# Kernel tuning notes

Measured on AMD Instinct MI355X. Metric: run time of the kernel, lower is better.

The kernel has to match this reference:

```python
import jax, jax.numpy as jnp
import numpy as np

N_C, N_E, IN_FEAT, OUT_FEAT = 8192, 8192, 256, 128


def setup_inputs() -> dict:
    key = jax.random.key(0)
    ks = jax.random.split(key, 9)
    s = 1.0 / np.sqrt(IN_FEAT)
    return {
        "emb_cause": jax.random.normal(ks[0], (N_C, IN_FEAT), jnp.float32),
        "emb_effect": jax.random.normal(ks[1], (N_E, IN_FEAT), jnp.float32),
        "causal_mask": jax.random.randint(ks[2], (N_C, N_E), 0, 2, jnp.int32),
        "Wq": jax.random.uniform(ks[3], (IN_FEAT, OUT_FEAT), jnp.float32, -s, s),
        "bq": jax.random.uniform(ks[4], (OUT_FEAT,), jnp.float32, -s, s),
        "Wk": jax.random.uniform(ks[5], (IN_FEAT, OUT_FEAT), jnp.float32, -s, s),
        "bk": jax.random.uniform(ks[6], (OUT_FEAT,), jnp.float32, -s, s),
        "Wv": jax.random.uniform(ks[7], (IN_FEAT, OUT_FEAT), jnp.float32, -s, s),
        "bv": jax.random.uniform(ks[8], (OUT_FEAT,), jnp.float32, -s, s),
    }


def reference(emb_cause, emb_effect, causal_mask, Wq, bq, Wk, bk, Wv, bv):
    Q = emb_cause @ Wq + bq          # [N_c, D]
    K = emb_effect @ Wk + bk         # [N_e, D]
    V = emb_effect @ Wv + bv         # [N_e, D]
    scale = 1.0 / jnp.sqrt(jnp.asarray(Q.shape[-1], Q.dtype))
    scores = (Q @ K.T) * scale       # [N_c, N_e]
    scores = jnp.where(causal_mask == 0, -jnp.inf, scores)
    attn_weights = jax.nn.softmax(scores, axis=-1)
    causal_output = attn_weights @ V  # [N_c, D]
    return causal_output, attn_weights
```

## Files before the change

### kernel.cpp

```cpp
#include <hip/hip_runtime.h>

#define NC   8192
#define NEFF 8192
#define DIN  256
#define DOUT 128
#define SCALE 0.08838834764831843f

typedef float  f32x4  __attribute__((ext_vector_type(4)));
typedef short  s16x8  __attribute__((ext_vector_type(8)));
typedef unsigned long long u64;

__device__ __forceinline__ short f2bf(float f) {
    unsigned int u = __builtin_bit_cast(unsigned int, f);
    u += 0x7FFFu + ((u >> 16) & 1u);
    return (short)(u >> 16);
}

__device__ __forceinline__ s16x8 ld8(const short* p) {
    return *(const s16x8*)__builtin_assume_aligned(p, 16);
}

__device__ __forceinline__ unsigned getdw(int4 v, int i) {
    switch (i & 3) {
        case 0: return (unsigned)v.x;
        case 1: return (unsigned)v.y;
        case 2: return (unsigned)v.z;
        default: return (unsigned)v.w;
    }
}


__global__ __launch_bounds__(256) void pack_kernel(
    const int* __restrict__ mask, u64* __restrict__ bm)
{
    const size_t stride = (size_t)gridDim.x * 256;
    const size_t i0 = (size_t)blockIdx.x * 256 + threadIdx.x;
    const bool lead = (threadIdx.x & 63) == 0;
    for (size_t i = i0; i < (size_t)NC * NEFF; i += 8 * stride) {
        int m[8];
#pragma unroll
        for (int j = 0; j < 8; j++) m[j] = mask[i + j * stride];
        u64 b[8];
#pragma unroll
        for (int j = 0; j < 8; j++) b[j] = __ballot(m[j] != 0);
        if (lead) {
#pragma unroll
            for (int j = 0; j < 8; j++) bm[(i + j * stride) >> 6] = b[j];
        }
    }
}

__global__ __launch_bounds__(256, 2) void qkv_kernel(
    const float* __restrict__ embc, const float* __restrict__ embe,
    const float* __restrict__ Wq, const float* __restrict__ bq,
    const float* __restrict__ Wk, const float* __restrict__ bk,
    const float* __restrict__ Wv, const float* __restrict__ bv,
    short* __restrict__ Qf, short* __restrict__ Kf, short* __restrict__ Vf)
{
    const int mat = blockIdx.y;
    const float* src  = (mat == 0) ? embc : embe;
    const float* W    = (mat == 0) ? Wq : (mat == 1 ? Wk : Wv);
    const float* bias = (mat == 0) ? bq : (mat == 1 ? bk : bv);

    __shared__ short wt[DOUT][136];
    __shared__ short tbuf[4][16][132];
    __shared__ short tbufV[128][68];

    const int tid  = threadIdx.x;
    const int wave = tid >> 6, lane = tid & 63;
    const int quad = lane >> 4, ln16 = lane & 15;
    const int rowbase = blockIdx.x * 64;
    const int arow = rowbase + wave * 16 + ln16;

    f32x4 acc[8];
#pragma unroll
    for (int i = 0; i < 8; i++) acc[i] = (f32x4){0.f, 0.f, 0.f, 0.f};

    for (int h = 0; h < 2; h++) {
        __syncthreads();
        {
            const int n0 = (tid & 31) * 4;
            const int kb = tid >> 5;
#pragma unroll
            for (int i = 0; i < 16; i++) {
                const int k = kb + i * 8;
                const float4 w4 = *(const float4*)(W + (size_t)(h * 128 + k) * DOUT + n0);
                wt[n0 + 0][k] = f2bf(w4.x);
                wt[n0 + 1][k] = f2bf(w4.y);
                wt[n0 + 2][k] = f2bf(w4.z);
                wt[n0 + 3][k] = f2bf(w4.w);
            }
        }
        __syncthreads();

        s16x8 afr[4];
#pragma unroll
        for (int kc = 0; kc < 4; kc++) {
            const float* ap = src + (size_t)arow * DIN + h * 128 + kc * 32 + quad * 8;
            const float4 a0 = *(const float4*)ap;
            const float4 a1 = *(const float4*)(ap + 4);
            s16x8 a;
            a[0] = f2bf(a0.x); a[1] = f2bf(a0.y); a[2] = f2bf(a0.z); a[3] = f2bf(a0.w);
            a[4] = f2bf(a1.x); a[5] = f2bf(a1.y); a[6] = f2bf(a1.z); a[7] = f2bf(a1.w);
            afr[kc] = a;
        }
#pragma unroll
        for (int nt = 0; nt < 8; nt++) {
#pragma unroll
            for (int kc = 0; kc < 4; kc++) {
                const s16x8 b = ld8(&wt[nt * 16 + ln16][kc * 32 + quad * 8]);
                acc[nt] = __builtin_amdgcn_mfma_f32_16x16x32_bf16(afr[kc], b, acc[nt], 0, 0, 0);
            }
        }
    }

    if (mat < 2) {
        short* dst = (mat == 0) ? Qf : Kf;
        const float sc = (mat == 0) ? SCALE : 1.0f;
#pragma unroll
        for (int nt = 0; nt < 8; nt++) {
            const float bb = bias[nt * 16 + ln16];
#pragma unroll
            for (int r = 0; r < 4; r++)
                tbuf[wave][quad * 4 + r][nt * 16 + ln16] = f2bf((acc[nt][r] + bb) * sc);
        }
        const int tile = blockIdx.x * 4 + wave;
#pragma unroll
        for (int kc = 0; kc < 4; kc++) {
            const s16x8 fr = ld8(&tbuf[wave][ln16][kc * 32 + quad * 8]);
            *(s16x8*)(dst + ((size_t)(tile * 4 + kc) * 64 + lane) * 8) = fr;
        }
    } else {
#pragma unroll
        for (int nt = 0; nt < 8; nt++) {
            const float bb = bias[nt * 16 + ln16];
#pragma unroll
            for (int r = 0; r < 4; r++)
                tbufV[nt * 16 + ln16][wave * 16 + quad * 4 + r] = f2bf(acc[nt][r] + bb);
        }
        __syncthreads();
        const int ct = blockIdx.x >> 1;
        const int ksub0 = (blockIdx.x & 1) * 2;
        const int ks = wave & 1;
#pragma unroll
        for (int t = 0; t < 4; t++) {
            const int nt2 = (wave >> 1) * 4 + t;
            const s16x8 fr = ld8(&tbufV[nt2 * 16 + ln16][ks * 32 + quad * 8]);
            *(s16x8*)(Vf + ((size_t)((ct * 8 + nt2) * 4 + ksub0 + ks) * 64 + lane) * 8) = fr;
        }
    }
}

__global__ __launch_bounds__(256, 4) void stats_kernel(
    const unsigned int* __restrict__ bm, const short* __restrict__ Qf,
    const short* __restrict__ Kf, float* __restrict__ lsum)
{
    const int bx = blockIdx.x, strip = blockIdx.y;
    const int tid  = threadIdx.x;
    const int wave = tid >> 6, lane = tid & 63;
    const int quad = lane >> 4, ln16 = lane & 15;
    const int rowbase = bx * 128 + wave * 32;
    const int t0 = rowbase >> 4;

    s16x8 aq[2][4];
#pragma unroll
    for (int rs = 0; rs < 2; rs++)
#pragma unroll
        for (int kc = 0; kc < 4; kc++)
            aq[rs][kc] = ld8(Qf + ((size_t)((t0 + rs) * 4 + kc) * 64 + lane) * 8);

    float lp[8] = {0.f, 0.f, 0.f, 0.f, 0.f, 0.f, 0.f, 0.f};

    for (int it = 0; it < 4; it++) {
        const int cb = strip * 512 + it * 128;

        int4 bmv[2][4];
#pragma unroll
        for (int rs = 0; rs < 2; rs++)
#pragma unroll
            for (int r = 0; r < 4; r++)
                bmv[rs][r] = *(const int4*)(bm + (size_t)(rowbase + rs * 16 + quad * 4 + r) * 256 + (cb >> 5));

#pragma unroll
        for (int nt = 0; nt < 8; nt++) {
            s16x8 bq[4];
#pragma unroll
            for (int kc = 0; kc < 4; kc++)
                bq[kc] = ld8(Kf + ((size_t)(((cb >> 4) + nt) * 4 + kc) * 64 + lane) * 8);
            f32x4 c0 = (f32x4){0.f, 0.f, 0.f, 0.f};
            f32x4 c1 = (f32x4){0.f, 0.f, 0.f, 0.f};
#pragma unroll
            for (int kc = 0; kc < 4; kc++) {
                c0 = __builtin_amdgcn_mfma_f32_16x16x32_bf16(aq[0][kc], bq[kc], c0, 0, 0, 0);
                c1 = __builtin_amdgcn_mfma_f32_16x16x32_bf16(aq[1][kc], bq[kc], c1, 0, 0, 0);
            }
#pragma unroll
            for (int rs = 0; rs < 2; rs++)
#pragma unroll
                for (int r = 0; r < 4; r++) {
                    const unsigned d = getdw(bmv[rs][r], nt >> 1);
                    const float cv = rs ? c1[r] : c0[r];
                    if ((d >> ((nt & 1) * 16 + ln16)) & 1u)
                        lp[rs * 4 + r] += __expf(cv);
                }
        }
    }

#pragma unroll
    for (int i = 0; i < 8; i++) {
        float v = lp[i];
        v += __shfl_xor(v, 1); v += __shfl_xor(v, 2);
        v += __shfl_xor(v, 4); v += __shfl_xor(v, 8);
        if (ln16 == 0)
            atomicAdd(&lsum[rowbase + (i >> 2) * 16 + quad * 4 + (i & 3)], v);
    }
}

__global__ __launch_bounds__(256, 4) void attn_kernel(
    const short* __restrict__ Qf, const short* __restrict__ Kf,
    const short* __restrict__ Vf, const float* __restrict__ lsum,
    const unsigned int* __restrict__ bm,
    float* __restrict__ outO, float* __restrict__ outW)
{
    __shared__ short wlds[4][16][132];

    const int bx = blockIdx.x, strip = blockIdx.y;
    const int tid  = threadIdx.x;
    const int wave = tid >> 6, lane = tid & 63;
    const int quad = lane >> 4, ln16 = lane & 15;
    const int rowbase = bx * 64 + wave * 16;
    const int t0 = rowbase >> 4;

    s16x8 aq[4];
#pragma unroll
    for (int kc = 0; kc < 4; kc++)
        aq[kc] = ld8(Qf + ((size_t)(t0 * 4 + kc) * 64 + lane) * 8);

    float rl[4];
#pragma unroll
    for (int r = 0; r < 4; r++)
        rl[r] = 1.0f / lsum[rowbase + quad * 4 + r];

    f32x4 o[8];
#pragma unroll
    for (int i = 0; i < 8; i++) o[i] = (f32x4){0.f, 0.f, 0.f, 0.f};

    for (int it = 0; it < 8; it++) {
        const int cb = strip * 1024 + it * 128;

        int4 bmv[4];
#pragma unroll
        for (int r = 0; r < 4; r++)
            bmv[r] = *(const int4*)(bm + (size_t)(rowbase + quad * 4 + r) * 256 + (cb >> 5));

#pragma unroll
        for (int nt = 0; nt < 8; nt++) {
            s16x8 bq[4];
#pragma unroll
            for (int kc = 0; kc < 4; kc++)
                bq[kc] = ld8(Kf + ((size_t)(((cb >> 4) + nt) * 4 + kc) * 64 + lane) * 8);
            f32x4 c = (f32x4){0.f, 0.f, 0.f, 0.f};
#pragma unroll
            for (int kc = 0; kc < 4; kc++)
                c = __builtin_amdgcn_mfma_f32_16x16x32_bf16(aq[kc], bq[kc], c, 0, 0, 0);
#pragma unroll
            for (int r = 0; r < 4; r++) {
                const int row = rowbase + quad * 4 + r;
                const unsigned d = getdw(bmv[r], nt >> 1);
                const float wv = ((d >> ((nt & 1) * 16 + ln16)) & 1u)
                                     ? __expf(c[r]) * rl[r] : 0.0f;
                outW[(size_t)row * NEFF + cb + nt * 16 + ln16] = wv;
                wlds[wave][quad * 4 + r][nt * 16 + ln16] = f2bf(wv);
            }
        }

#pragma unroll
        for (int ks = 0; ks < 4; ks++) {
            const s16x8 aw = ld8(&wlds[wave][ln16][ks * 32 + quad * 8]);
#pragma unroll
            for (int nt2 = 0; nt2 < 8; nt2++) {
                const s16x8 bv = ld8(Vf + ((size_t)(((cb >> 7) * 8 + nt2) * 4 + ks) * 64 + lane) * 8);
                o[nt2] = __builtin_amdgcn_mfma_f32_16x16x32_bf16(aw, bv, o[nt2], 0, 0, 0);
            }
        }
    }

#pragma unroll
    for (int nt2 = 0; nt2 < 8; nt2++)
#pragma unroll
        for (int r = 0; r < 4; r++) {
            const int row = rowbase + quad * 4 + r;
            atomicAdd(&outO[(size_t)row * DOUT + nt2 * 16 + ln16], o[nt2][r]);
        }
}

extern "C" void kernel_launch(void* const* d_in, const int* in_sizes, int n_in,
                              void* d_out, int out_size, void* d_ws, size_t ws_size,
                              hipStream_t stream) {
    (void)in_sizes; (void)n_in; (void)out_size; (void)ws_size;

    const float* embc = (const float*)d_in[0];
    const float* embe = (const float*)d_in[1];
    const int*   mask = (const int*)d_in[2];
    const float* Wq = (const float*)d_in[3];
    const float* bq = (const float*)d_in[4];
    const float* Wk = (const float*)d_in[5];
    const float* bk = (const float*)d_in[6];
    const float* Wv = (const float*)d_in[7];
    const float* bv = (const float*)d_in[8];

    char* ws = (char*)d_ws;
    short* Qf = (short*)(ws);
    short* Kf = (short*)(ws + (2u << 20));
    short* Vf = (short*)(ws + (4u << 20));
    float* lsum = (float*)(ws + (6u << 20));
    unsigned int* bm = (unsigned int*)(ws + (8u << 20));

    float* outO = (float*)d_out;
    float* outW = outO + (size_t)NC * DOUT;

    hipMemsetAsync(lsum, 0, NC * sizeof(float), stream);
    hipMemsetAsync(outO, 0, (size_t)NC * DOUT * sizeof(float), stream);

    pack_kernel<<<8192, 256, 0, stream>>>(mask, (u64*)bm);
    qkv_kernel<<<dim3(128, 3), 256, 0, stream>>>(embc, embe, Wq, bq, Wk, bk, Wv, bv,
                                                 Qf, Kf, Vf);
    stats_kernel<<<dim3(64, 16), 256, 0, stream>>>(bm, Qf, Kf, lsum);
    attn_kernel<<<dim3(128, 8), 256, 0, stream>>>(Qf, Kf, Vf, lsum, bm, outO, outW);
}
```

Before: 659.9 us.

## Fuse mask bit-packing into stats kernel and drop separate pack pass

Removes the standalone pack_kernel. Each stats block now reads its own 128x512 tile of the int32 mask, ballots it into a bitmask held in LDS, and writes that bitmask to global memory for attn_kernel. It then reads mask bits from LDS instead of global memory. This saves one kernel launch and one extra global round trip of the bitmask, in exchange for more LDS use and a serial packing phase at the start of each stats block.

Result: slower. 751.5 us (+13.9%).

```diff
diff --git a/kernel.cpp b/kernel.cpp
--- a/kernel.cpp
+++ b/kernel.cpp
@@ -29,26 +29,6 @@
     }
 }
 
-
-__global__ __launch_bounds__(256) void pack_kernel(
-    const int* __restrict__ mask, u64* __restrict__ bm)
-{
-    const size_t stride = (size_t)gridDim.x * 256;
-    const size_t i0 = (size_t)blockIdx.x * 256 + threadIdx.x;
-    const bool lead = (threadIdx.x & 63) == 0;
-    for (size_t i = i0; i < (size_t)NC * NEFF; i += 8 * stride) {
-        int m[8];
-#pragma unroll
-        for (int j = 0; j < 8; j++) m[j] = mask[i + j * stride];
-        u64 b[8];
-#pragma unroll
-        for (int j = 0; j < 8; j++) b[j] = __ballot(m[j] != 0);
-        if (lead) {
-#pragma unroll
-            for (int j = 0; j < 8; j++) bm[(i + j * stride) >> 6] = b[j];
-        }
-    }
-}
 
 __global__ __launch_bounds__(256, 2) void qkv_kernel(
     const float* __restrict__ embc, const float* __restrict__ embe,
@@ -152,14 +132,49 @@
 }
 
 __global__ __launch_bounds__(256, 4) void stats_kernel(
-    const unsigned int* __restrict__ bm, const short* __restrict__ Qf,
-    const short* __restrict__ Kf, float* __restrict__ lsum)
+    const int* __restrict__ mask, const short* __restrict__ Qf,
+    const short* __restrict__ Kf, float* __restrict__ lsum,
+    u64* __restrict__ bmG)
 {
+    __shared__ u64 lds_bm[128][8];
+
     const int bx = blockIdx.x, strip = blockIdx.y;
     const int tid  = threadIdx.x;
     const int wave = tid >> 6, lane = tid & 63;
     const int quad = lane >> 4, ln16 = lane & 15;
-    const int rowbase = bx * 128 + wave * 32;
+    const int blkrow = bx * 128;
+    const int cb0 = strip * 512;
+
+    for (int i = 0; i < 256; i += 8) {
+        int mv[8];
+#pragma unroll
+        for (int j = 0; j < 8; j++) {
+            const int t = (i + j) * 4 + wave;
+            mv[j] = mask[(size_t)(blkrow + (t >> 3)) * NEFF + cb0 + (t & 7) * 64 + lane];
+        }
+        u64 lb[8];
+#pragma unroll
+        for (int j = 0; j < 8; j++) lb[j] = __ballot(mv[j] != 0);
+        if (lane == 0) {
+#pragma unroll
+            for (int j = 0; j < 8; j++) {
+                const int t = (i + j) * 4 + wave;
+                lds_bm[t >> 3][t & 7] = lb[j];
+            }
+        }
+    }
+    __syncthreads();
+
+    {
+        const int r = tid >> 1, half = tid & 1;
+        const int4* src = (const int4*)&lds_bm[r][half * 4];
+        int4* dst = (int4*)(bmG + (size_t)(blkrow + r) * 128 + strip * 8 + half * 4);
+        dst[0] = src[0];
+        dst[1] = src[1];
+    }
+
+    const int rowbase = blkrow + wave * 32;
+    const int wrow = wave * 32;
     const int t0 = rowbase >> 4;
 
     s16x8 aq[2][4];
@@ -172,14 +187,15 @@
     float lp[8] = {0.f, 0.f, 0.f, 0.f, 0.f, 0.f, 0.f, 0.f};
 
     for (int it = 0; it < 4; it++) {
-        const int cb = strip * 512 + it * 128;
+        const int cb = cb0 + it * 128;
 
         int4 bmv[2][4];
 #pragma unroll
         for (int rs = 0; rs < 2; rs++)
 #pragma unroll
             for (int r = 0; r < 4; r++)
-                bmv[rs][r] = *(const int4*)(bm + (size_t)(rowbase + rs * 16 + quad * 4 + r) * 256 + (cb >> 5));
+                bmv[rs][r] = *(const int4*)((const char*)lds_bm
+                               + (size_t)(wrow + rs * 16 + quad * 4 + r) * 64 + it * 16);
 
 #pragma unroll
         for (int nt = 0; nt < 8; nt++) {
@@ -322,9 +338,8 @@
     hipMemsetAsync(lsum, 0, NC * sizeof(float), stream);
     hipMemsetAsync(outO, 0, (size_t)NC * DOUT * sizeof(float), stream);
 
-    pack_kernel<<<8192, 256, 0, stream>>>(mask, (u64*)bm);
     qkv_kernel<<<dim3(128, 3), 256, 0, stream>>>(embc, embe, Wq, bq, Wk, bk, Wv, bv,
                                                  Qf, Kf, Vf);
-    stats_kernel<<<dim3(64, 16), 256, 0, stream>>>(bm, Qf, Kf, lsum);
+    stats_kernel<<<dim3(64, 16), 256, 0, stream>>>(mask, Qf, Kf, lsum, (u64*)bm);
     attn_kernel<<<dim3(128, 8), 256, 0, stream>>>(Qf, Kf, Vf, lsum, bm, outO, outW);
 }
```
